# Performance work log

Measured on AMD Instinct MI355X. Metric: run time of the kernel, lower is better.

The kernel has to match this reference:

```python
import jax, jax.numpy as jnp
import numpy as np
import math

DIM = 768
FFN_DIM = 4 * DIM
EPS = 1e-5

def layer_norm(x, gamma, beta):
    mu = jnp.mean(x, axis=-1, keepdims=True)
    var = jnp.var(x, axis=-1, keepdims=True)
    return (x - mu) * jax.lax.rsqrt(var + EPS) * gamma + beta

def setup_inputs() -> dict:
    key = jax.random.key(0)
    ks = jax.random.split(key, 8)
    b, n, d = 8, 2048, DIM
    s = 1.0 / math.sqrt(d)
    x = jax.random.normal(ks[0], (b, n, d), dtype=jnp.float32)
    Wq = jax.random.normal(ks[1], (d, d), dtype=jnp.float32) * s
    Wk = jax.random.normal(ks[2], (d, d), dtype=jnp.float32) * s
    Wv = jax.random.normal(ks[3], (d, d), dtype=jnp.float32) * s
    W1 = jax.random.normal(ks[4], (d, FFN_DIM), dtype=jnp.float32) * s
    b1 = jnp.zeros((FFN_DIM,), dtype=jnp.float32)
    W2 = jax.random.normal(ks[5], (FFN_DIM, d), dtype=jnp.float32) * (1.0 / math.sqrt(FFN_DIM))
    b2 = jnp.zeros((d,), dtype=jnp.float32)
    g1 = jnp.ones((d,), dtype=jnp.float32); be1 = jnp.zeros((d,), dtype=jnp.float32)
    g2 = jnp.ones((d,), dtype=jnp.float32); be2 = jnp.zeros((d,), dtype=jnp.float32)
    return {"x": x, "Wq": Wq, "Wk": Wk, "Wv": Wv, "ln1_g": g1, "ln1_b": be1,
            "W1": W1, "b1": b1, "W2": W2, "b2": b2, "ln2_g": g2, "ln2_b": be2}

def reference(x, Wq, Wk, Wv, ln1_g, ln1_b, W1, b1, W2, b2, ln2_g, ln2_b):
    # Self-attention (single head, full dim; dropout in eval mode => identity)
    Q = jnp.einsum('bnd,de->bne', x, Wq)
    K = jnp.einsum('bnd,de->bne', x, Wk)
    V = jnp.einsum('bnd,de->bne', x, Wv)
    scores = jnp.einsum('bnd,bmd->bnm', Q, K) / math.sqrt(DIM)  # [b,n,n]
    attn = jax.nn.softmax(scores, axis=-1)
    O = jnp.einsum('bnm,bmd->bnd', attn, V)
    h = layer_norm(x + O, ln1_g, ln1_b)
    # FFN with exact GELU (torch nn.GELU default)
    hidden = jax.nn.gelu(jnp.einsum('bnd,df->bnf', h, W1) + b1, approximate=False)
    out = jnp.einsum('bnf,fd->bnd', hidden, W2) + b2
    return layer_norm(h + out, ln2_g, ln2_b)
```

## Files before the change

kernel.cpp:

```cpp
#include <hip/hip_runtime.h>
#include <hip/hip_bf16.h>
#include <math.h>

using u16 = unsigned short;
typedef __bf16 bf16x8 __attribute__((ext_vector_type(8)));
typedef float f32x4 __attribute__((ext_vector_type(4)));
typedef u16 u16x8 __attribute__((ext_vector_type(8)));

__device__ __forceinline__ u16 f2b(float f) {
  union { float f; unsigned u; } c; c.f = f;
  unsigned r = c.u + 0x7fffu + ((c.u >> 16) & 1u);
  return (u16)(r >> 16);
}
__device__ __forceinline__ float b2f(u16 h) {
  union { unsigned u; float f; } c; c.u = ((unsigned)h) << 16;
  return c.f;
}

__device__ __forceinline__ float fast_gelu(float t) {
  float y = fminf(1.5957691216f * t + 0.07135481283f * t * t * t, 80.f);
  float e = __expf(y);
  return t * e * (1.0f / (e + 1.0f));
}

#define EPI_BF16 0
#define EPI_BF16_SCALE 1
#define EPI_GELU_BIAS 2
#define EPI_F32_BIAS 3

#define GLDS16(src, dst)                                                     \
  __builtin_amdgcn_global_load_lds(                                          \
      (const __attribute__((address_space(1))) void*)(src),                  \
      (__attribute__((address_space(3))) void*)(dst), 16, 0, 0)

__device__ __forceinline__ int xswz(int o, int n) {
  int q = n >> 3, r = n & 7, x = o & 7, i = o >> 3;
  return (x < r ? x * (q + 1) : r * (q + 1) + (x - r) * q) + i;
}

template <int EPI>
__device__ __forceinline__ void epi_store(
    void* Cg, const float* bias, float v, long long off, int ccol, float scale)
{
  if (EPI == EPI_BF16) {
    ((u16*)Cg)[off] = f2b(v);
  } else if (EPI == EPI_BF16_SCALE) {
    ((u16*)Cg)[off] = f2b(v * scale);
  } else if (EPI == EPI_GELU_BIAS) {
    ((u16*)Cg)[off] = f2b(fast_gelu(v + bias[ccol]));
  } else {
    ((float*)Cg)[off] = v + bias[ccol];
  }
}

template <int EPI>
__global__ __launch_bounds__(256, 2) void gemm_ring(
    const u16* __restrict__ Ag, const u16* __restrict__ Bg,
    void* __restrict__ Cg, const float* __restrict__ bias,
    int nbx, int K, float scale, int lda, int ldb, int ldc,
    long long sAz, long long sBz, long long sCz)
{
  __shared__ __align__(16) u16 lds[32768];

  const int tid = threadIdx.x;
  const int wave = tid >> 6, lane = tid & 63;
  const int wr = wave >> 1, wc = wave & 1;
  const int id = xswz(blockIdx.x, gridDim.x);
  const int bx = id % nbx, by = id / nbx;
  const int m0 = by * 128, n0 = bx * 128;
  const long long z = blockIdx.z;
  const u16* A = Ag + z * sAz + (long long)m0 * lda;
  const u16* B = Bg + z * sBz + (long long)n0 * ldb;

  const int rA = wave * 32 + (lane >> 2);
  const int slot4 = (lane & 3) ^ ((rA >> 1) & 3);
  const u16* a0 = A + (long long)rA * lda + slot4 * 8;
  const u16* a1 = a0 + (long long)16 * lda;
  const u16* b0 = B + (long long)rA * ldb + slot4 * 8;
  const u16* b1 = b0 + (long long)16 * ldb;
  const int dw = wave * 1024;

  int offA[4], offB[4];
#pragma unroll
  for (int f = 0; f < 4; ++f) {
    int ra = wr * 64 + f * 16 + (lane & 15);
    int ba = ra * 64 + ((lane >> 4) << 4);
    offA[f] = ba ^ (((ba >> 7) & 3) << 4);
    int rb = wc * 64 + f * 16 + (lane & 15);
    int bb = rb * 64 + ((lane >> 4) << 4);
    offB[f] = bb ^ (((bb >> 7) & 3) << 4);
  }

  f32x4 acc[4][4];
#pragma unroll
  for (int m = 0; m < 4; ++m)
#pragma unroll
    for (int n = 0; n < 4; ++n) acc[m][n] = f32x4{0.f, 0.f, 0.f, 0.f};

  const char* ldsc = (const char*)lds;
  const int NH = K >> 5;

#pragma unroll
  for (int s = 0; s < 3; ++s) {
    const int kc = s * 32;
    GLDS16(a0 + kc, lds + s * 8192 + dw);
    GLDS16(a1 + kc, lds + s * 8192 + dw + 512);
    GLDS16(b0 + kc, lds + s * 8192 + 4096 + dw);
    GLDS16(b1 + kc, lds + s * 8192 + 4096 + dw + 512);
  }
  asm volatile("s_waitcnt vmcnt(8)" ::: "memory");
  asm volatile("s_barrier" ::: "memory");

#pragma unroll 4
  for (int h = 0; h < NH; ++h) {
    const int hp = (h + 3 < NH) ? h + 3 : h + 3 - NH;
    const int sw = (h + 3) & 3;
    const int kc = hp << 5;
    GLDS16(a0 + kc, lds + sw * 8192 + dw);
    GLDS16(a1 + kc, lds + sw * 8192 + dw + 512);
    GLDS16(b0 + kc, lds + sw * 8192 + 4096 + dw);
    GLDS16(b1 + kc, lds + sw * 8192 + 4096 + dw + 512);

    const char* pA = ldsc + (h & 3) * 16384;
    const char* pB = pA + 8192;
    bf16x8 Af[4], Bf[4];
#pragma unroll
    for (int m = 0; m < 4; ++m) Af[m] = *(const bf16x8*)(pA + offA[m]);
#pragma unroll
    for (int n = 0; n < 4; ++n) Bf[n] = *(const bf16x8*)(pB + offB[n]);
    __builtin_amdgcn_s_setprio(1);
#pragma unroll
    for (int m = 0; m < 4; ++m)
#pragma unroll
      for (int n = 0; n < 4; ++n)
        acc[m][n] = __builtin_amdgcn_mfma_f32_16x16x32_bf16(Af[m], Bf[n], acc[m][n], 0, 0, 0);
    __builtin_amdgcn_s_setprio(0);
    asm volatile("s_waitcnt vmcnt(8)" ::: "memory");
    asm volatile("s_barrier" ::: "memory");
  }

#pragma unroll
  for (int mf = 0; mf < 4; ++mf) {
#pragma unroll
    for (int nf = 0; nf < 4; ++nf) {
      const int crow = m0 + wr * 64 + mf * 16 + (lane >> 4) * 4;
      const int ccol = n0 + wc * 64 + nf * 16 + (lane & 15);
#pragma unroll
      for (int j = 0; j < 4; ++j) {
        const long long off = (long long)(crow + j) * ldc + ccol + z * sCz;
        epi_store<EPI>(Cg, bias, acc[mf][nf][j], off, ccol, scale);
      }
    }
  }
}

__global__ __launch_bounds__(256) void cast_f32_bf16(
    const float* __restrict__ x, u16* __restrict__ y, long long n4)
{
  const long long i = (long long)blockIdx.x * 256 + threadIdx.x;
  if (i >= n4) return;
  const float4 v = ((const float4*)x)[i];
  ushort4 o;
  o.x = f2b(v.x); o.y = f2b(v.y); o.z = f2b(v.z); o.w = f2b(v.w);
  ((ushort4*)y)[i] = o;
}

template <bool SRC_BF16>
__global__ __launch_bounds__(256) void transpose_cast(
    const void* __restrict__ srcv, u16* __restrict__ dst, int R, int C, int ldsrc,
    long long szSrc, long long szDst)
{
  __shared__ float tile[32][33];
  const long long zs = (long long)blockIdx.z * szSrc;
  const long long zd = (long long)blockIdx.z * szDst;
  const int c0 = blockIdx.x * 32, r0 = blockIdx.y * 32;
  const int tx = threadIdx.x & 31, ty = threadIdx.x >> 5;
#pragma unroll
  for (int i = 0; i < 4; ++i) {
    const int r = r0 + ty + i * 8;
    float v;
    if (SRC_BF16) v = b2f(((const u16*)srcv)[zs + (long long)r * ldsrc + c0 + tx]);
    else          v = ((const float*)srcv)[zs + (long long)r * ldsrc + c0 + tx];
    tile[ty + i * 8][tx] = v;
  }
  __syncthreads();
#pragma unroll
  for (int i = 0; i < 4; ++i) {
    const int c = c0 + ty + i * 8;
    dst[zd + (long long)c * R + r0 + tx] = f2b(tile[tx][ty + i * 8]);
  }
}

__global__ __launch_bounds__(256) void softmax_rows(
    u16* __restrict__ S, int ncol)
{
  __shared__ float red[8];
  const long long row = blockIdx.x;
  u16* s = S + row * ncol;
  const int t = threadIdx.x;

  const u16x8 u = *(const u16x8*)&s[t * 8];
  float v[8];
#pragma unroll
  for (int j = 0; j < 8; ++j) v[j] = b2f(u[j]);

  float mx = v[0];
#pragma unroll
  for (int j = 1; j < 8; ++j) mx = fmaxf(mx, v[j]);
  for (int o = 32; o; o >>= 1) mx = fmaxf(mx, __shfl_xor(mx, o));
  if ((t & 63) == 0) red[t >> 6] = mx;
  __syncthreads();
  mx = fmaxf(fmaxf(red[0], red[1]), fmaxf(red[2], red[3]));

  float sum = 0.f;
#pragma unroll
  for (int j = 0; j < 8; ++j) { v[j] = __expf(v[j] - mx); sum += v[j]; }
  for (int o = 32; o; o >>= 1) sum += __shfl_xor(sum, o);
  if ((t & 63) == 0) red[4 + (t >> 6)] = sum;
  __syncthreads();
  sum = red[4] + red[5] + red[6] + red[7];

  const float inv = 1.0f / sum;
  u16x8 o8;
#pragma unroll
  for (int j = 0; j < 8; ++j) o8[j] = f2b(v[j] * inv);
  *(u16x8*)&s[t * 8] = o8;
}

__global__ __launch_bounds__(256) void ln1_kernel(
    const float* __restrict__ x, const u16* __restrict__ O,
    const float* __restrict__ g, const float* __restrict__ be,
    u16* __restrict__ h)
{
  __shared__ float red[8];
  const long long row = blockIdx.x;
  const float* xr = x + row * 768;
  const u16* orow = O + row * 768;
  const int t = threadIdx.x, base = t * 3;

  float v[3];
#pragma unroll
  for (int j = 0; j < 3; ++j) v[j] = xr[base + j] + b2f(orow[base + j]);
  float s = v[0] + v[1] + v[2];
  float ss = v[0] * v[0] + v[1] * v[1] + v[2] * v[2];
  for (int o = 32; o; o >>= 1) { s += __shfl_xor(s, o); ss += __shfl_xor(ss, o); }
  if ((t & 63) == 0) { red[t >> 6] = s; red[4 + (t >> 6)] = ss; }
  __syncthreads();
  s = red[0] + red[1] + red[2] + red[3];
  ss = red[4] + red[5] + red[6] + red[7];
  const float mu = s * (1.0f / 768.0f);
  const float var = ss * (1.0f / 768.0f) - mu * mu;
  const float inv = rsqrtf(var + 1e-5f);
#pragma unroll
  for (int j = 0; j < 3; ++j) {
    const float o = (v[j] - mu) * inv * g[base + j] + be[base + j];
    h[row * 768 + base + j] = f2b(o);
  }
}

__global__ __launch_bounds__(256) void ln2_kernel(
    const u16* __restrict__ h, const float* __restrict__ oflt,
    const float* __restrict__ g, const float* __restrict__ be,
    float* __restrict__ y)
{
  __shared__ float red[8];
  const long long row = blockIdx.x;
  const u16* hr = h + row * 768;
  const float* orow = oflt + row * 768;
  const int t = threadIdx.x, base = t * 3;

  float v[3];
#pragma unroll
  for (int j = 0; j < 3; ++j) v[j] = b2f(hr[base + j]) + orow[base + j];
  float s = v[0] + v[1] + v[2];
  float ss = v[0] * v[0] + v[1] * v[1] + v[2] * v[2];
  for (int o = 32; o; o >>= 1) { s += __shfl_xor(s, o); ss += __shfl_xor(ss, o); }
  if ((t & 63) == 0) { red[t >> 6] = s; red[4 + (t >> 6)] = ss; }
  __syncthreads();
  s = red[0] + red[1] + red[2] + red[3];
  ss = red[4] + red[5] + red[6] + red[7];
  const float mu = s * (1.0f / 768.0f);
  const float var = ss * (1.0f / 768.0f) - mu * mu;
  const float inv = rsqrtf(var + 1e-5f);
#pragma unroll
  for (int j = 0; j < 3; ++j) {
    y[row * 768 + base + j] = (v[j] - mu) * inv * g[base + j] + be[base + j];
  }
}

extern "C" void kernel_launch(void* const* d_in, const int* in_sizes, int n_in,
                              void* d_out, int out_size, void* d_ws, size_t ws_size,
                              hipStream_t stream)
{
  const int Bb = 8, Nn = 2048, D = 768, F = 3072, E = 2304;
  const int M = Bb * Nn;
  const long long MD = (long long)M * D;

  const float* x   = (const float*)d_in[0];
  const float* Wq  = (const float*)d_in[1];
  const float* Wk  = (const float*)d_in[2];
  const float* Wv  = (const float*)d_in[3];
  const float* g1  = (const float*)d_in[4];
  const float* be1 = (const float*)d_in[5];
  const float* W1  = (const float*)d_in[6];
  const float* b1  = (const float*)d_in[7];
  const float* W2  = (const float*)d_in[8];
  const float* b2  = (const float*)d_in[9];
  const float* g2  = (const float*)d_in[10];
  const float* be2 = (const float*)d_in[11];

  u16* xb    = (u16*)d_out;
  u16* wqkvt = xb + MD;
  u16* wqt = wqkvt;
  u16* wkt = wqkvt + 768 * 768;
  u16* wvt = wqkvt + 2 * 768 * 768;

  char* w = (char*)d_ws;
  size_t off = 0;
  auto alloc = [&](size_t bytes) { void* p = w + off; off += bytes; return p; };
  u16* w1t = (u16*)alloc((size_t)F * D * 2);
  u16* w2t = (u16*)alloc((size_t)D * F * 2);
  u16* hb  = (u16*)alloc((size_t)MD * 2);
  u16* qkv = (u16*)alloc((size_t)M * E * 2);
  u16* Vt  = (u16*)alloc((size_t)Bb * D * Nn * 2);
  u16* S   = (u16*)alloc((size_t)Bb * Nn * Nn * 2);
  u16* O   = (u16*)alloc((size_t)MD * 2);
  u16*   hidden = qkv;
  float* outf   = (float*)S;

  const dim3 tcb(256);
  const float scl = 0.03608439182435161f;

  cast_f32_bf16<<<(unsigned)(MD / 4 / 256), 256, 0, stream>>>(x, xb, MD / 4);
  transpose_cast<false><<<dim3(D / 32, D / 32, 1), tcb, 0, stream>>>(Wq, wqt, D, D, D, 0, 0);
  transpose_cast<false><<<dim3(D / 32, D / 32, 1), tcb, 0, stream>>>(Wk, wkt, D, D, D, 0, 0);
  transpose_cast<false><<<dim3(D / 32, D / 32, 1), tcb, 0, stream>>>(Wv, wvt, D, D, D, 0, 0);
  transpose_cast<false><<<dim3(F / 32, D / 32, 1), tcb, 0, stream>>>(W1, w1t, D, F, F, 0, 0);
  transpose_cast<false><<<dim3(D / 32, F / 32, 1), tcb, 0, stream>>>(W2, w2t, F, D, D, 0, 0);

  gemm_ring<EPI_BF16><<<dim3(18 * 128, 1, 1), 256, 0, stream>>>(
      xb, wqkvt, qkv, nullptr, 18, D, 1.f, D, D, E, 0, 0, 0);

  transpose_cast<true><<<dim3(D / 32, Nn / 32, Bb), tcb, 0, stream>>>(
      qkv + 1536, Vt, Nn, D, E, (long long)Nn * E, (long long)D * Nn);

  gemm_ring<EPI_BF16_SCALE><<<dim3(16 * 16, 1, Bb), 256, 0, stream>>>(
      qkv, qkv + 768, S, nullptr, 16, D, scl, E, E, Nn,
      (long long)Nn * E, (long long)Nn * E, (long long)Nn * Nn);

  softmax_rows<<<M, 256, 0, stream>>>(S, Nn);

  gemm_ring<EPI_BF16><<<dim3(6 * 16, 1, Bb), 256, 0, stream>>>(
      S, Vt, O, nullptr, 6, Nn, 1.f, Nn, Nn, D,
      (long long)Nn * Nn, (long long)D * Nn, (long long)Nn * D);

  ln1_kernel<<<M, 256, 0, stream>>>(x, O, g1, be1, hb);

  gemm_ring<EPI_GELU_BIAS><<<dim3(24 * 128, 1, 1), 256, 0, stream>>>(
      hb, w1t, hidden, b1, 24, D, 1.f, D, D, F, 0, 0, 0);

  gemm_ring<EPI_F32_BIAS><<<dim3(6 * 128, 1, 1), 256, 0, stream>>>(
      hidden, w2t, outf, b2, 6, F, 1.f, F, F, D, 0, 0, 0);

  ln2_kernel<<<M, 256, 0, stream>>>(hb, outf, g2, be2, (float*)d_out);
}
```

Before: 548.8 us.

## Double-buffer GEMM with 64-wide K steps, compute V transposed directly, bf16 FFN output

The GEMM main loop changes from a 4-stage ring of 32-wide K slices to a double-buffered loop over 64-wide K tiles, each split into two 32-wide halves with extra barriers. The QKV projection now produces only Q and K. V is computed already transposed by a separate GEMM (Wv^T times x), which removes the transpose_cast pass over V. The FFN second GEMM now writes a bf16 output instead of fp32, halving the traffic into LN2 at some cost in precision. The new pipeline issues more barriers per K step and keeps less prefetch depth than the ring.

Measured after the change: 525.1 us. 1.05x faster.

```diff
diff --git a/kernel.cpp b/kernel.cpp
--- a/kernel.cpp
+++ b/kernel.cpp
@@ -27,6 +27,7 @@
 #define EPI_BF16_SCALE 1
 #define EPI_GELU_BIAS 2
 #define EPI_F32_BIAS 3
+#define EPI_BF16_BIAS 4
 
 #define GLDS16(src, dst)                                                     \
   __builtin_amdgcn_global_load_lds(                                          \
@@ -48,13 +49,15 @@
     ((u16*)Cg)[off] = f2b(v * scale);
   } else if (EPI == EPI_GELU_BIAS) {
     ((u16*)Cg)[off] = f2b(fast_gelu(v + bias[ccol]));
+  } else if (EPI == EPI_F32_BIAS) {
+    ((float*)Cg)[off] = v + bias[ccol];
   } else {
-    ((float*)Cg)[off] = v + bias[ccol];
+    ((u16*)Cg)[off] = f2b(v + bias[ccol]);
   }
 }
 
 template <int EPI>
-__global__ __launch_bounds__(256, 2) void gemm_ring(
+__global__ __launch_bounds__(256, 2) void gemm128(
     const u16* __restrict__ Ag, const u16* __restrict__ Bg,
     void* __restrict__ Cg, const float* __restrict__ bias,
     int nbx, int K, float scale, int lda, int ldb, int ldc,
@@ -73,12 +76,13 @@
   const u16* B = Bg + z * sBz + (long long)n0 * ldb;
 
   const int rA = wave * 32 + (lane >> 2);
-  const int slot4 = (lane & 3) ^ ((rA >> 1) & 3);
-  const u16* a0 = A + (long long)rA * lda + slot4 * 8;
+  const int slot = (lane & 3) ^ ((rA >> 1) & 3);
+  const u16* a0 = A + (long long)rA * lda + slot * 8;
   const u16* a1 = a0 + (long long)16 * lda;
-  const u16* b0 = B + (long long)rA * ldb + slot4 * 8;
+  const u16* b0 = B + (long long)rA * ldb + slot * 8;
   const u16* b1 = b0 + (long long)16 * ldb;
-  const int dw = wave * 1024;
+  const int d0 = wave * 32 * 32;
+  const int d1 = (wave * 32 + 16) * 32;
 
   int offA[4], offB[4];
 #pragma unroll
@@ -98,36 +102,33 @@
     for (int n = 0; n < 4; ++n) acc[m][n] = f32x4{0.f, 0.f, 0.f, 0.f};
 
   const char* ldsc = (const char*)lds;
-  const int NH = K >> 5;
-
-#pragma unroll
-  for (int s = 0; s < 3; ++s) {
-    const int kc = s * 32;
-    GLDS16(a0 + kc, lds + s * 8192 + dw);
-    GLDS16(a1 + kc, lds + s * 8192 + dw + 512);
-    GLDS16(b0 + kc, lds + s * 8192 + 4096 + dw);
-    GLDS16(b1 + kc, lds + s * 8192 + 4096 + dw + 512);
-  }
-  asm volatile("s_waitcnt vmcnt(8)" ::: "memory");
+  const int NT = K >> 6;
+
+  GLDS16(a0, lds + 0 * 4096 + d0);  GLDS16(a1, lds + 0 * 4096 + d1);
+  GLDS16(b0, lds + 2 * 4096 + d0);  GLDS16(b1, lds + 2 * 4096 + d1);
+  GLDS16(a0 + 32, lds + 1 * 4096 + d0);  GLDS16(a1 + 32, lds + 1 * 4096 + d1);
+  GLDS16(b0 + 32, lds + 3 * 4096 + d0);  GLDS16(b1 + 32, lds + 3 * 4096 + d1);
+  asm volatile("s_waitcnt vmcnt(4)" ::: "memory");
   asm volatile("s_barrier" ::: "memory");
 
-#pragma unroll 4
-  for (int h = 0; h < NH; ++h) {
-    const int hp = (h + 3 < NH) ? h + 3 : h + 3 - NH;
-    const int sw = (h + 3) & 3;
-    const int kc = hp << 5;
-    GLDS16(a0 + kc, lds + sw * 8192 + dw);
-    GLDS16(a1 + kc, lds + sw * 8192 + dw + 512);
-    GLDS16(b0 + kc, lds + sw * 8192 + 4096 + dw);
-    GLDS16(b1 + kc, lds + sw * 8192 + 4096 + dw + 512);
-
-    const char* pA = ldsc + (h & 3) * 16384;
-    const char* pB = pA + 8192;
+  for (int t = 0; t < NT; ++t) {
+    const int buf = t & 1, nb = buf ^ 1;
+    const int kc = (t + 1 < NT) ? ((t + 1) << 6) : 0;
+    const char* pA0 = ldsc + (buf * 4 + 0) * 8192;
+    const char* pA1 = ldsc + (buf * 4 + 1) * 8192;
+    const char* pB0 = ldsc + (buf * 4 + 2) * 8192;
+    const char* pB1 = ldsc + (buf * 4 + 3) * 8192;
+    u16* q = lds + nb * 4 * 4096;
+
     bf16x8 Af[4], Bf[4];
-#pragma unroll
-    for (int m = 0; m < 4; ++m) Af[m] = *(const bf16x8*)(pA + offA[m]);
-#pragma unroll
-    for (int n = 0; n < 4; ++n) Bf[n] = *(const bf16x8*)(pB + offB[n]);
+
+    GLDS16(a0 + kc, q + 0 * 4096 + d0);  GLDS16(a1 + kc, q + 0 * 4096 + d1);
+    GLDS16(b0 + kc, q + 2 * 4096 + d0);  GLDS16(b1 + kc, q + 2 * 4096 + d1);
+#pragma unroll
+    for (int m = 0; m < 4; ++m) Af[m] = *(const bf16x8*)(pA0 + offA[m]);
+#pragma unroll
+    for (int n = 0; n < 4; ++n) Bf[n] = *(const bf16x8*)(pB0 + offB[n]);
+    asm volatile("s_barrier" ::: "memory");
     __builtin_amdgcn_s_setprio(1);
 #pragma unroll
     for (int m = 0; m < 4; ++m)
@@ -135,7 +136,24 @@
       for (int n = 0; n < 4; ++n)
         acc[m][n] = __builtin_amdgcn_mfma_f32_16x16x32_bf16(Af[m], Bf[n], acc[m][n], 0, 0, 0);
     __builtin_amdgcn_s_setprio(0);
-    asm volatile("s_waitcnt vmcnt(8)" ::: "memory");
+    asm volatile("s_waitcnt vmcnt(4)" ::: "memory");
+    asm volatile("s_barrier" ::: "memory");
+
+    GLDS16(a0 + kc + 32, q + 1 * 4096 + d0);  GLDS16(a1 + kc + 32, q + 1 * 4096 + d1);
+    GLDS16(b0 + kc + 32, q + 3 * 4096 + d0);  GLDS16(b1 + kc + 32, q + 3 * 4096 + d1);
+#pragma unroll
+    for (int m = 0; m < 4; ++m) Af[m] = *(const bf16x8*)(pA1 + offA[m]);
+#pragma unroll
+    for (int n = 0; n < 4; ++n) Bf[n] = *(const bf16x8*)(pB1 + offB[n]);
+    asm volatile("s_barrier" ::: "memory");
+    __builtin_amdgcn_s_setprio(1);
+#pragma unroll
+    for (int m = 0; m < 4; ++m)
+#pragma unroll
+      for (int n = 0; n < 4; ++n)
+        acc[m][n] = __builtin_amdgcn_mfma_f32_16x16x32_bf16(Af[m], Bf[n], acc[m][n], 0, 0, 0);
+    __builtin_amdgcn_s_setprio(0);
+    asm volatile("s_waitcnt vmcnt(4)" ::: "memory");
     asm volatile("s_barrier" ::: "memory");
   }
 
@@ -259,19 +277,19 @@
 }
 
 __global__ __launch_bounds__(256) void ln2_kernel(
-    const u16* __restrict__ h, const float* __restrict__ oflt,
+    const u16* __restrict__ h, const u16* __restrict__ ob,
     const float* __restrict__ g, const float* __restrict__ be,
     float* __restrict__ y)
 {
   __shared__ float red[8];
   const long long row = blockIdx.x;
   const u16* hr = h + row * 768;
-  const float* orow = oflt + row * 768;
+  const u16* orow = ob + row * 768;
   const int t = threadIdx.x, base = t * 3;
 
   float v[3];
 #pragma unroll
-  for (int j = 0; j < 3; ++j) v[j] = b2f(hr[base + j]) + orow[base + j];
+  for (int j = 0; j < 3; ++j) v[j] = b2f(hr[base + j]) + b2f(orow[base + j]);
   float s = v[0] + v[1] + v[2];
   float ss = v[0] * v[0] + v[1] * v[1] + v[2] * v[2];
   for (int o = 32; o; o >>= 1) { s += __shfl_xor(s, o); ss += __shfl_xor(ss, o); }
@@ -292,7 +310,7 @@
                               void* d_out, int out_size, void* d_ws, size_t ws_size,
                               hipStream_t stream)
 {
-  const int Bb = 8, Nn = 2048, D = 768, F = 3072, E = 2304;
+  const int Bb = 8, Nn = 2048, D = 768, F = 3072, E = 1536;
   const int M = Bb * Nn;
   const long long MD = (long long)M * D;
 
@@ -309,11 +327,9 @@
   const float* g2  = (const float*)d_in[10];
   const float* be2 = (const float*)d_in[11];
 
-  u16* xb    = (u16*)d_out;
-  u16* wqkvt = xb + MD;
-  u16* wqt = wqkvt;
-  u16* wkt = wqkvt + 768 * 768;
-  u16* wvt = wqkvt + 2 * 768 * 768;
+  u16* xb   = (u16*)d_out;
+  u16* wqkt = xb + MD;
+  u16* wvt  = wqkt + (size_t)E * D;
 
   char* w = (char*)d_ws;
   size_t off = 0;
@@ -321,45 +337,46 @@
   u16* w1t = (u16*)alloc((size_t)F * D * 2);
   u16* w2t = (u16*)alloc((size_t)D * F * 2);
   u16* hb  = (u16*)alloc((size_t)MD * 2);
-  u16* qkv = (u16*)alloc((size_t)M * E * 2);
+  u16* qk  = (u16*)alloc((size_t)M * E * 2);
   u16* Vt  = (u16*)alloc((size_t)Bb * D * Nn * 2);
   u16* S   = (u16*)alloc((size_t)Bb * Nn * Nn * 2);
   u16* O   = (u16*)alloc((size_t)MD * 2);
-  u16*   hidden = qkv;
-  float* outf   = (float*)S;
+  u16* hidden = qk;
+  u16* outf   = qk + (size_t)M * F;
 
   const dim3 tcb(256);
   const float scl = 0.03608439182435161f;
 
   cast_f32_bf16<<<(unsigned)(MD / 4 / 256), 256, 0, stream>>>(x, xb, MD / 4);
-  transpose_cast<false><<<dim3(D / 32, D / 32, 1), tcb, 0, stream>>>(Wq, wqt, D, D, D, 0, 0);
-  transpose_cast<false><<<dim3(D / 32, D / 32, 1), tcb, 0, stream>>>(Wk, wkt, D, D, D, 0, 0);
+  transpose_cast<false><<<dim3(D / 32, D / 32, 1), tcb, 0, stream>>>(Wq, wqkt, D, D, D, 0, 0);
+  transpose_cast<false><<<dim3(D / 32, D / 32, 1), tcb, 0, stream>>>(Wk, wqkt + D * D, D, D, D, 0, 0);
   transpose_cast<false><<<dim3(D / 32, D / 32, 1), tcb, 0, stream>>>(Wv, wvt, D, D, D, 0, 0);
   transpose_cast<false><<<dim3(F / 32, D / 32, 1), tcb, 0, stream>>>(W1, w1t, D, F, F, 0, 0);
   transpose_cast<false><<<dim3(D / 32, F / 32, 1), tcb, 0, stream>>>(W2, w2t, F, D, D, 0, 0);
 
-  gemm_ring<EPI_BF16><<<dim3(18 * 128, 1, 1), 256, 0, stream>>>(
-      xb, wqkvt, qkv, nullptr, 18, D, 1.f, D, D, E, 0, 0, 0);
-
-  transpose_cast<true><<<dim3(D / 32, Nn / 32, Bb), tcb, 0, stream>>>(
-      qkv + 1536, Vt, Nn, D, E, (long long)Nn * E, (long long)D * Nn);
-
-  gemm_ring<EPI_BF16_SCALE><<<dim3(16 * 16, 1, Bb), 256, 0, stream>>>(
-      qkv, qkv + 768, S, nullptr, 16, D, scl, E, E, Nn,
+  gemm128<EPI_BF16><<<dim3(12 * 128, 1, 1), 256, 0, stream>>>(
+      xb, wqkt, qk, nullptr, 12, D, 1.f, D, D, E, 0, 0, 0);
+
+  gemm128<EPI_BF16><<<dim3(16 * 6, 1, Bb), 256, 0, stream>>>(
+      wvt, xb, Vt, nullptr, 16, D, 1.f, D, D, Nn,
+      0, (long long)Nn * D, (long long)D * Nn);
+
+  gemm128<EPI_BF16_SCALE><<<dim3(16 * 16, 1, Bb), 256, 0, stream>>>(
+      qk, qk + D, S, nullptr, 16, D, scl, E, E, Nn,
       (long long)Nn * E, (long long)Nn * E, (long long)Nn * Nn);
 
   softmax_rows<<<M, 256, 0, stream>>>(S, Nn);
 
-  gemm_ring<EPI_BF16><<<dim3(6 * 16, 1, Bb), 256, 0, stream>>>(
+  gemm128<EPI_BF16><<<dim3(6 * 16, 1, Bb), 256, 0, stream>>>(
       S, Vt, O, nullptr, 6, Nn, 1.f, Nn, Nn, D,
       (long long)Nn * Nn, (long long)D * Nn, (long long)Nn * D);
 
   ln1_kernel<<<M, 256, 0, stream>>>(x, O, g1, be1, hb);
 
-  gemm_ring<EPI_GELU_BIAS><<<dim3(24 * 128, 1, 1), 256, 0, stream>>>(
+  gemm128<EPI_GELU_BIAS><<<dim3(24 * 128, 1, 1), 256, 0, stream>>>(
       hb, w1t, hidden, b1, 24, D, 1.f, D, D, F, 0, 0, 0);
 
-  gemm_ring<EPI_F32_BIAS><<<dim3(6 * 128, 1, 1), 256, 0, stream>>>(
+  gemm128<EPI_BF16_BIAS><<<dim3(6 * 128, 1, 1), 256, 0, stream>>>(
       hidden, w2t, outf, b2, 6, F, 1.f, F, F, D, 0, 0, 0);
 
   ln2_kernel<<<M, 256, 0, stream>>>(hb, outf, g2, be2, (float*)d_out);
```
